# Kernel optimization log

Hardware: AMD Instinct MI355X
Metric: run time of the kernel (lower is better)

The kernel has to match this reference:

```python
import jax, jax.numpy as jnp
import numpy as np

EPS = 1e-8  # matches torch F.cosine_similarity eps


def setup_inputs() -> dict:
    key = jax.random.key(0)
    k1, k2, k3 = jax.random.split(key, 3)
    S, B, H = 16, 512, 2048
    OGLogits = jax.random.normal(k1, (B, H), dtype=jnp.float32)
    enhancedSamplesLogits = jax.random.normal(k2, (S, B, H), dtype=jnp.float32)
    W = jax.random.normal(k3, (H, H), dtype=jnp.float32) * (1.0 / np.sqrt(H))
    b = jnp.zeros((H,), dtype=jnp.float32)
    return {"OGLogits": OGLogits, "enhancedSamplesLogits": enhancedSamplesLogits, "W": W, "b": b}


def reference(OGLogits, enhancedSamplesLogits, W, b):
    # Original torch code builds the full (S*B, B) cosine-similarity matrix and
    # keeps only the diagonal via an eye mask; mathematically that equals the
    # per-pair cosine similarity cos(enhanced[s,b], OG[b]), computed directly here.
    e_norm = jnp.linalg.norm(enhancedSamplesLogits, axis=-1)          # (S, B)
    o_norm = jnp.linalg.norm(OGLogits, axis=-1)                       # (B,)
    dots = jnp.einsum('sbh,bh->sb', enhancedSamplesLogits, OGLogits)  # (S, B)
    sims = dots / jnp.maximum(e_norm * o_norm[None, :], EPS)          # (S, B)
    weighted = enhancedSamplesLogits * sims[..., None]                # (S, B, H)
    weightedRep = weighted.mean(axis=0)                               # (B, H)
    return weightedRep @ W.T + b                                      # (B, H)
```

## Files before the change

### kernel.cpp

```cpp
#include <hip/hip_runtime.h>

#define S_DIM 16
#define B_DIM 512
#define H_DIM 2048
#define EPS 1e-8f

typedef short bf16x8 __attribute__((ext_vector_type(8)));
typedef float f32x4 __attribute__((ext_vector_type(4)));

__device__ __forceinline__ unsigned short f2bf(float f) {
    union { float f; unsigned int u; } v; v.f = f;
    unsigned int u = v.u;
    unsigned int r = (u + 0x7fffu + ((u >> 16) & 1u)) >> 16;
    return (unsigned short)r;
}

__device__ __forceinline__ float dot4(const float4& a, const float4& b) {
    return a.x*b.x + a.y*b.y + a.z*b.z + a.w*b.w;
}

__global__ __launch_bounds__(512, 4) void simwrep_kernel(
    const float* __restrict__ OG, const float* __restrict__ E,
    unsigned short* __restrict__ wrep) {
    const int b = blockIdx.x;
    const int t = threadIdx.x;
    const int lane = t & 63;
    const int wave = t >> 6;

    __shared__ float4 ogs[512];
    __shared__ float4 buf[8][512];
    __shared__ float red[8];

    const float4* og4 = (const float4*)(OG + (size_t)b * H_DIM);
    float4 o = og4[t];
    ogs[t] = o;
    float p = dot4(o, o);
    #pragma unroll
    for (int m = 32; m >= 1; m >>= 1) p += __shfl_xor(p, m, 64);
    if (lane == 0) red[wave] = p;
    __syncthreads();
    float og2 = 0.f;
    #pragma unroll
    for (int w = 0; w < 8; ++w) og2 += red[w];
    const float onorm = sqrtf(og2);

    float4 acc[8];
    #pragma unroll
    for (int i = 0; i < 8; ++i) acc[i] = make_float4(0.f, 0.f, 0.f, 0.f);

    #pragma unroll
    for (int si = 0; si < 2; ++si) {
        const int s = wave + si * 8;
        const float4* e4 = (const float4*)(E + ((size_t)s * B_DIM + b) * H_DIM);
        float4 e[8];
        float d = 0.f, n = 0.f;
        #pragma unroll
        for (int i = 0; i < 8; ++i) {
            e[i] = e4[i * 64 + lane];
            float4 og = ogs[i * 64 + lane];
            d += dot4(e[i], og);
            n += dot4(e[i], e[i]);
        }
        #pragma unroll
        for (int m = 32; m >= 1; m >>= 1) {
            d += __shfl_xor(d, m, 64);
            n += __shfl_xor(n, m, 64);
        }
        const float sim = d / fmaxf(sqrtf(n) * onorm, EPS);
        #pragma unroll
        for (int i = 0; i < 8; ++i) {
            acc[i].x += e[i].x * sim; acc[i].y += e[i].y * sim;
            acc[i].z += e[i].z * sim; acc[i].w += e[i].w * sim;
        }
    }

    #pragma unroll
    for (int i = 0; i < 8; ++i) buf[wave][i * 64 + lane] = acc[i];
    __syncthreads();

    float4 s = buf[0][t];
    #pragma unroll
    for (int w = 1; w < 8; ++w) {
        float4 v = buf[w][t];
        s.x += v.x; s.y += v.y; s.z += v.z; s.w += v.w;
    }
    const float sc = 1.f / (float)S_DIM;
    ushort4 ob;
    ob.x = f2bf(s.x * sc); ob.y = f2bf(s.y * sc);
    ob.z = f2bf(s.z * sc); ob.w = f2bf(s.w * sc);
    ((ushort4*)wrep)[(size_t)b * (H_DIM / 4) + t] = ob;
}

__global__ __launch_bounds__(256) void gemm_kernel(
    const unsigned short* __restrict__ A, const float* __restrict__ W,
    const float* __restrict__ bias, float* __restrict__ out) {
    const int n0 = blockIdx.x * 64;
    const int m0 = blockIdx.y * 64;

    __shared__ unsigned short As[64][72];
    __shared__ unsigned short Ws[64][72];

    const int t = threadIdx.x;
    const int lane = t & 63;
    const int wave = t >> 6;
    const int wm = (wave & 1) * 32;
    const int wn = (wave >> 1) * 32;
    const int lr = t >> 2;
    const int lq = t & 3;

    const unsigned short* ap = A + (size_t)(m0 + lr) * H_DIM + lq * 16;
    const float* wp = W + (size_t)(n0 + lr) * H_DIM + lq * 16;

    f32x4 acc00 = {0.f, 0.f, 0.f, 0.f};
    f32x4 acc01 = {0.f, 0.f, 0.f, 0.f};
    f32x4 acc10 = {0.f, 0.f, 0.f, 0.f};
    f32x4 acc11 = {0.f, 0.f, 0.f, 0.f};

    const int row = lane & 15;
    const int q = lane >> 4;

    uint4 av0 = *(const uint4*)(ap);
    uint4 av1 = *(const uint4*)(ap + 8);
    float4 wv0 = *(const float4*)(wp);
    float4 wv1 = *(const float4*)(wp + 4);
    float4 wv2 = *(const float4*)(wp + 8);
    float4 wv3 = *(const float4*)(wp + 12);

    for (int k0 = 0; k0 < H_DIM; k0 += 64) {
        *(uint4*)&As[lr][lq * 16] = av0;
        *(uint4*)&As[lr][lq * 16 + 8] = av1;
        ushort4 c0, c1, c2, c3;
        c0.x = f2bf(wv0.x); c0.y = f2bf(wv0.y); c0.z = f2bf(wv0.z); c0.w = f2bf(wv0.w);
        c1.x = f2bf(wv1.x); c1.y = f2bf(wv1.y); c1.z = f2bf(wv1.z); c1.w = f2bf(wv1.w);
        c2.x = f2bf(wv2.x); c2.y = f2bf(wv2.y); c2.z = f2bf(wv2.z); c2.w = f2bf(wv2.w);
        c3.x = f2bf(wv3.x); c3.y = f2bf(wv3.y); c3.z = f2bf(wv3.z); c3.w = f2bf(wv3.w);
        *(ushort4*)&Ws[lr][lq * 16]      = c0;
        *(ushort4*)&Ws[lr][lq * 16 + 4]  = c1;
        *(ushort4*)&Ws[lr][lq * 16 + 8]  = c2;
        *(ushort4*)&Ws[lr][lq * 16 + 12] = c3;
        __syncthreads();
        if (k0 + 64 < H_DIM) {
            av0 = *(const uint4*)(ap + k0 + 64);
            av1 = *(const uint4*)(ap + k0 + 72);
            wv0 = *(const float4*)(wp + k0 + 64);
            wv1 = *(const float4*)(wp + k0 + 68);
            wv2 = *(const float4*)(wp + k0 + 72);
            wv3 = *(const float4*)(wp + k0 + 76);
        }
        #pragma unroll
        for (int ks = 0; ks < 2; ++ks) {
            bf16x8 a0 = *(const bf16x8*)&As[wm + row][ks * 32 + q * 8];
            bf16x8 a1 = *(const bf16x8*)&As[wm + 16 + row][ks * 32 + q * 8];
            bf16x8 b0 = *(const bf16x8*)&Ws[wn + row][ks * 32 + q * 8];
            bf16x8 b1 = *(const bf16x8*)&Ws[wn + 16 + row][ks * 32 + q * 8];
            acc00 = __builtin_amdgcn_mfma_f32_16x16x32_bf16(a0, b0, acc00, 0, 0, 0);
            acc01 = __builtin_amdgcn_mfma_f32_16x16x32_bf16(a0, b1, acc01, 0, 0, 0);
            acc10 = __builtin_amdgcn_mfma_f32_16x16x32_bf16(a1, b0, acc10, 0, 0, 0);
            acc11 = __builtin_amdgcn_mfma_f32_16x16x32_bf16(a1, b1, acc11, 0, 0, 0);
        }
        __syncthreads();
    }

    const int col = lane & 15;
    const float bias0 = bias[n0 + wn + col];
    const float bias1 = bias[n0 + wn + 16 + col];
    #pragma unroll
    for (int r = 0; r < 4; ++r) {
        const int mr = q * 4 + r;
        float* o0 = out + (size_t)(m0 + wm + mr) * H_DIM + n0 + wn;
        float* o1 = out + (size_t)(m0 + wm + 16 + mr) * H_DIM + n0 + wn;
        o0[col]      = acc00[r] + bias0;
        o0[16 + col] = acc01[r] + bias1;
        o1[col]      = acc10[r] + bias0;
        o1[16 + col] = acc11[r] + bias1;
    }
}

extern "C" void kernel_launch(void* const* d_in, const int* in_sizes, int n_in,
                              void* d_out, int out_size, void* d_ws, size_t ws_size,
                              hipStream_t stream) {
    const float* OG   = (const float*)d_in[0];
    const float* E    = (const float*)d_in[1];
    const float* W    = (const float*)d_in[2];
    const float* bias = (const float*)d_in[3];
    float* out = (float*)d_out;

    unsigned short* wrep = (unsigned short*)d_ws;

    simwrep_kernel<<<B_DIM, 512, 0, stream>>>(OG, E, wrep);
    gemm_kernel<<<dim3(H_DIM / 64, B_DIM / 64), 256, 0, stream>>>(wrep, W, bias, out);
}
```

Before: 139.0 us.

## Pre-convert W to bf16 in the similarity kernel and stream bf16 into GEMM

The first kernel now also converts the fp32 weight matrix to bf16 once, with each block converting four rows, and writes it to workspace. The GEMM then loads bf16 weight tiles directly instead of re-reading fp32 W and converting it in every tile loop. Each W tile is read by 8 row-blocks, so this halves W traffic in the GEMM and removes repeated conversion ALU work. In exchange it adds a 16 MB read and 8 MB write to the first kernel. The per-wave accumulators also move from registers to shared memory and the occupancy hint is dropped, which lowers register pressure.

```diff
diff --git a/kernel.cpp b/kernel.cpp
--- a/kernel.cpp
+++ b/kernel.cpp
@@ -19,9 +19,10 @@
     return a.x*b.x + a.y*b.y + a.z*b.z + a.w*b.w;
 }
 
-__global__ __launch_bounds__(512, 4) void simwrep_kernel(
+__global__ __launch_bounds__(512) void simwrep_kernel(
     const float* __restrict__ OG, const float* __restrict__ E,
-    unsigned short* __restrict__ wrep) {
+    const float* __restrict__ W, unsigned short* __restrict__ wrep,
+    unsigned short* __restrict__ Wb) {
     const int b = blockIdx.x;
     const int t = threadIdx.x;
     const int lane = t & 63;
@@ -44,10 +45,6 @@
     for (int w = 0; w < 8; ++w) og2 += red[w];
     const float onorm = sqrtf(og2);
 
-    float4 acc[8];
-    #pragma unroll
-    for (int i = 0; i < 8; ++i) acc[i] = make_float4(0.f, 0.f, 0.f, 0.f);
-
     #pragma unroll
     for (int si = 0; si < 2; ++si) {
         const int s = wave + si * 8;
@@ -67,15 +64,24 @@
             n += __shfl_xor(n, m, 64);
         }
         const float sim = d / fmaxf(sqrtf(n) * onorm, EPS);
-        #pragma unroll
-        for (int i = 0; i < 8; ++i) {
-            acc[i].x += e[i].x * sim; acc[i].y += e[i].y * sim;
-            acc[i].z += e[i].z * sim; acc[i].w += e[i].w * sim;
+        if (si == 0) {
+            #pragma unroll
+            for (int i = 0; i < 8; ++i) {
+                float4 v;
+                v.x = e[i].x * sim; v.y = e[i].y * sim;
+                v.z = e[i].z * sim; v.w = e[i].w * sim;
+                buf[wave][i * 64 + lane] = v;
+            }
+        } else {
+            #pragma unroll
+            for (int i = 0; i < 8; ++i) {
+                float4 v = buf[wave][i * 64 + lane];
+                v.x += e[i].x * sim; v.y += e[i].y * sim;
+                v.z += e[i].z * sim; v.w += e[i].w * sim;
+                buf[wave][i * 64 + lane] = v;
+            }
         }
     }
-
-    #pragma unroll
-    for (int i = 0; i < 8; ++i) buf[wave][i * 64 + lane] = acc[i];
     __syncthreads();
 
     float4 s = buf[0][t];
@@ -89,10 +95,20 @@
     ob.x = f2bf(s.x * sc); ob.y = f2bf(s.y * sc);
     ob.z = f2bf(s.z * sc); ob.w = f2bf(s.w * sc);
     ((ushort4*)wrep)[(size_t)b * (H_DIM / 4) + t] = ob;
+
+    const float4* w4 = (const float4*)W;
+    #pragma unroll
+    for (int j = 0; j < 4; ++j) {
+        const size_t idx = (size_t)b * 2048 + j * 512 + t;
+        float4 v = w4[idx];
+        ushort4 c;
+        c.x = f2bf(v.x); c.y = f2bf(v.y); c.z = f2bf(v.z); c.w = f2bf(v.w);
+        ((ushort4*)Wb)[idx] = c;
+    }
 }
 
 __global__ __launch_bounds__(256) void gemm_kernel(
-    const unsigned short* __restrict__ A, const float* __restrict__ W,
+    const unsigned short* __restrict__ A, const unsigned short* __restrict__ Wb,
     const float* __restrict__ bias, float* __restrict__ out) {
     const int n0 = blockIdx.x * 64;
     const int m0 = blockIdx.y * 64;
@@ -109,7 +125,7 @@
     const int lq = t & 3;
 
     const unsigned short* ap = A + (size_t)(m0 + lr) * H_DIM + lq * 16;
-    const float* wp = W + (size_t)(n0 + lr) * H_DIM + lq * 16;
+    const unsigned short* bp = Wb + (size_t)(n0 + lr) * H_DIM + lq * 16;
 
     f32x4 acc00 = {0.f, 0.f, 0.f, 0.f};
     f32x4 acc01 = {0.f, 0.f, 0.f, 0.f};
@@ -121,31 +137,20 @@
 
     uint4 av0 = *(const uint4*)(ap);
     uint4 av1 = *(const uint4*)(ap + 8);
-    float4 wv0 = *(const float4*)(wp);
-    float4 wv1 = *(const float4*)(wp + 4);
-    float4 wv2 = *(const float4*)(wp + 8);
-    float4 wv3 = *(const float4*)(wp + 12);
+    uint4 bv0 = *(const uint4*)(bp);
+    uint4 bv1 = *(const uint4*)(bp + 8);
 
     for (int k0 = 0; k0 < H_DIM; k0 += 64) {
-        *(uint4*)&As[lr][lq * 16] = av0;
+        *(uint4*)&As[lr][lq * 16]     = av0;
         *(uint4*)&As[lr][lq * 16 + 8] = av1;
-        ushort4 c0, c1, c2, c3;
-        c0.x = f2bf(wv0.x); c0.y = f2bf(wv0.y); c0.z = f2bf(wv0.z); c0.w = f2bf(wv0.w);
-        c1.x = f2bf(wv1.x); c1.y = f2bf(wv1.y); c1.z = f2bf(wv1.z); c1.w = f2bf(wv1.w);
-        c2.x = f2bf(wv2.x); c2.y = f2bf(wv2.y); c2.z = f2bf(wv2.z); c2.w = f2bf(wv2.w);
-        c3.x = f2bf(wv3.x); c3.y = f2bf(wv3.y); c3.z = f2bf(wv3.z); c3.w = f2bf(wv3.w);
-        *(ushort4*)&Ws[lr][lq * 16]      = c0;
-        *(ushort4*)&Ws[lr][lq * 16 + 4]  = c1;
-        *(ushort4*)&Ws[lr][lq * 16 + 8]  = c2;
-        *(ushort4*)&Ws[lr][lq * 16 + 12] = c3;
+        *(uint4*)&Ws[lr][lq * 16]     = bv0;
+        *(uint4*)&Ws[lr][lq * 16 + 8] = bv1;
         __syncthreads();
         if (k0 + 64 < H_DIM) {
             av0 = *(const uint4*)(ap + k0 + 64);
             av1 = *(const uint4*)(ap + k0 + 72);
-            wv0 = *(const float4*)(wp + k0 + 64);
-            wv1 = *(const float4*)(wp + k0 + 68);
-            wv2 = *(const float4*)(wp + k0 + 72);
-            wv3 = *(const float4*)(wp + k0 + 76);
+            bv0 = *(const uint4*)(bp + k0 + 64);
+            bv1 = *(const uint4*)(bp + k0 + 72);
         }
         #pragma unroll
         for (int ks = 0; ks < 2; ++ks) {
@@ -186,7 +191,8 @@
     float* out = (float*)d_out;
 
     unsigned short* wrep = (unsigned short*)d_ws;
+    unsigned short* Wb   = wrep + (size_t)B_DIM * H_DIM;
 
-    simwrep_kernel<<<B_DIM, 512, 0, stream>>>(OG, E, wrep);
-    gemm_kernel<<<dim3(H_DIM / 64, B_DIM / 64), 256, 0, stream>>>(wrep, W, bias, out);
+    simwrep_kernel<<<B_DIM, 512, 0, stream>>>(OG, E, W, wrep, Wb);
+    gemm_kernel<<<dim3(H_DIM / 64, B_DIM / 64), 256, 0, stream>>>(wrep, Wb, bias, out);
 }
```

New measurement: 128.6 us. -7.5%, faster.
